# Optimization experiments

Hardware: AMD Instinct MI355X
Metric: run time of the kernel (lower is better)

## Reference

```python
import jax, jax.numpy as jnp
import numpy as np

B, N, F_IN, F_OUT = 8, 2048, 128, 64
ALPHA = 0.2  # LeakyReLU negative slope
NEG_INF = -9e15


def setup_inputs() -> dict:
    key = jax.random.key(0)
    k1, k2, k3, k4 = jax.random.split(key, 4)
    h = jax.random.normal(k1, (B, N, F_IN), dtype=jnp.float32)
    adj = jax.random.randint(k2, (B, N, N), 0, 2, dtype=jnp.int32)
    # xavier_uniform with gain=1.414 approximated by scaled normals (values are arbitrary params)
    W = jax.random.normal(k3, (F_IN, F_OUT), dtype=jnp.float32) * (1.414 * np.sqrt(2.0 / (F_IN + F_OUT)))
    a = jax.random.normal(k4, (2 * F_OUT, 1), dtype=jnp.float32) * (1.414 * np.sqrt(2.0 / (2 * F_OUT + 1)))
    return {"h": h, "adj": adj, "W": W, "a": a}


def reference(h, adj, W, a):
    # Wh: [B, N, F_out]
    Wh = jnp.einsum('bnf,fo->bno', h, W)
    Fo = W.shape[1]
    a1 = a[:Fo, 0]   # [F_out]
    a2 = a[Fo:, 0]   # [F_out]
    # e[b,i,j] = leakyrelu(Wh[b,i]@a1 + Wh[b,j]@a2)  (== cat(Wh_i,Wh_j)@a, same math, no N^2*2F blowup)
    e1 = jnp.einsum('bno,o->bn', Wh, a1)  # [B, N]
    e2 = jnp.einsum('bno,o->bn', Wh, a2)  # [B, N]
    e = e1[:, :, None] + e2[:, None, :]   # [B, N, N]
    e = jnp.where(e > 0, e, ALPHA * e)    # LeakyReLU
    e = jnp.where(adj > 0, e, NEG_INF)    # mask non-edges
    attention = jax.nn.softmax(e, axis=-1)
    # dropout is identity in inference mode (deterministic reference)
    h_prime = jnp.einsum('bij,bjo->bio', attention, Wh)  # [B, N, F_out]
    return jax.nn.elu(h_prime)  # concat=True branch
```

## Files before the change

kernel.cpp:

```cpp
#include <hip/hip_runtime.h>
#include <hip/hip_bf16.h>

#define BB 8
#define NN 2048
#define FIN 128
#define FO 64
#define ALPHA 0.2f

typedef __attribute__((ext_vector_type(8))) short bf16x8;
typedef __attribute__((ext_vector_type(4))) float f32x4;
typedef __attribute__((ext_vector_type(4))) int i32x4;

typedef __attribute__((address_space(1))) const void gvoid;
typedef __attribute__((address_space(3))) void lvoid;

__device__ inline void gl_lds16(const void* g, void* l) {
    __builtin_amdgcn_global_load_lds((gvoid*)g, (lvoid*)l, 16, 0, 0);
}

__device__ inline short f2bf(float x) {
    unsigned u = __float_as_uint(x);
    u += 0x7fffu + ((u >> 16) & 1u);
    return (short)(u >> 16);
}

__global__ __launch_bounds__(256) void wh_kernel(
    const float* __restrict__ h, const float* __restrict__ W,
    const float* __restrict__ a, float* __restrict__ e1, float* __restrict__ e2,
    short* __restrict__ whF)
{
    __shared__ float hs[32][FIN];
    const int r0 = blockIdx.x * 32;
    const int t = threadIdx.x;
    const float4* hsrc = (const float4*)(h + (size_t)r0 * FIN);
    float4* hdst = (float4*)(&hs[0][0]);
#pragma unroll
    for (int k = 0; k < 4; k++) hdst[t + 256 * k] = hsrc[t + 256 * k];
    __syncthreads();

    const int o = t & 63;
    const int wv = t >> 6;
    float acc[8];
#pragma unroll
    for (int rr = 0; rr < 8; rr++) acc[rr] = 0.f;

    for (int f = 0; f < FIN; f += 4) {
        const float w0 = W[(f + 0) * FO + o];
        const float w1 = W[(f + 1) * FO + o];
        const float w2 = W[(f + 2) * FO + o];
        const float w3 = W[(f + 3) * FO + o];
#pragma unroll
        for (int rr = 0; rr < 8; rr++) {
            float4 hv = *(const float4*)&hs[wv * 8 + rr][f];
            acc[rr] = fmaf(hv.x, w0, acc[rr]);
            acc[rr] = fmaf(hv.y, w1, acc[rr]);
            acc[rr] = fmaf(hv.z, w2, acc[rr]);
            acc[rr] = fmaf(hv.w, w3, acc[rr]);
        }
    }

    const int b   = r0 / NN;
    const int ib0 = r0 - b * NN;
    const int ibb = ib0 + wv * 8;
    const int jc  = ibb >> 5;
    const int qq  = (ibb >> 3) & 3;
    const int ot  = o >> 4, mm = o & 15;
    const int L   = mm + qq * 16;
    bf16x8 frag;
#pragma unroll
    for (int rr = 0; rr < 8; rr++) frag[rr] = f2bf(acc[rr]);
    *(bf16x8*)(whF + ((((size_t)(b * 64 + jc) * 4 + ot) * 64 + L) * 8)) = frag;

    const float a1 = a[o], a2 = a[FO + o];
#pragma unroll
    for (int rr = 0; rr < 8; rr++) {
        float v1 = acc[rr] * a1, v2 = acc[rr] * a2;
#pragma unroll
        for (int msk = 32; msk >= 1; msk >>= 1) {
            v1 += __shfl_xor(v1, msk, 64);
            v2 += __shfl_xor(v2, msk, 64);
        }
        if (o == 0) { e1[r0 + wv * 8 + rr] = v1; e2[r0 + wv * 8 + rr] = v2; }
    }
}

__global__ __launch_bounds__(256) void e2max_kernel(
    const float* __restrict__ e2, float* __restrict__ e2max)
{
    const int b = blockIdx.x;
    const int t = threadIdx.x;
    float m = -1e30f;
    for (int j = t; j < NN; j += 256) m = fmaxf(m, e2[b * NN + j]);
#pragma unroll
    for (int k = 32; k >= 1; k >>= 1) m = fmaxf(m, __shfl_xor(m, k, 64));
    __shared__ float red[4];
    if ((t & 63) == 0) red[t >> 6] = m;
    __syncthreads();
    if (t == 0) e2max[b] = fmaxf(fmaxf(red[0], red[1]), fmaxf(red[2], red[3]));
}

struct SMemS { int adj[16][260]; float e2[256]; };
struct SMemC { float comb[4][16][64]; float lsum[4][16]; };
union SMemU { SMemS s; SMemC c; };

__global__ __launch_bounds__(256) void attn_kernel(
    const int* __restrict__ adj, const float* __restrict__ e1,
    const float* __restrict__ e2, const float* __restrict__ e2max,
    const short* __restrict__ whF, float* __restrict__ out)
{
    __shared__ SMemU sm;
    const int t = threadIdx.x, w = t >> 6, lane = t & 63;
    const int m = lane & 15, q = lane >> 4;
    const int blk = blockIdx.x;
    const int b  = blk >> 7;
    const int i0 = (blk & 127) * 16;
    const int i  = i0 + m;

    const float e1v = e1[b * NN + i];
    float mi = e1v + e2max[b];
    mi = mi > 0.f ? mi : ALPHA * mi;

    const short* whFb = whF + (size_t)b * (64 * 4 * 64 * 8);
    const int* arow0 = adj + ((size_t)(b * NN + i0)) * NN + lane * 4;
    const float* e2g = e2 + b * NN + lane * 4;

    f32x4 acc0 = {0.f,0.f,0.f,0.f}, acc1 = acc0, acc2 = acc0, acc3 = acc0;
    float lsum = 0.f;

    for (int j0 = 0; j0 < NN; j0 += 256) {
#pragma unroll
        for (int k = 0; k < 4; k++) {
            const int r = w * 4 + k;
            gl_lds16(arow0 + (size_t)r * NN + j0, &sm.s.adj[r][0]);
        }
        if (w == 0) gl_lds16(e2g + j0, &sm.s.e2[0]);
        __syncthreads();

#pragma unroll
        for (int s2 = 0; s2 < 2; s2++) {
            const int col = w * 64 + s2 * 32 + q * 8;
            i32x4 a0 = *(const i32x4*)&sm.s.adj[m][col];
            i32x4 a1 = *(const i32x4*)&sm.s.adj[m][col + 4];
            f32x4 ev0 = *(const f32x4*)&sm.s.e2[col];
            f32x4 ev1 = *(const f32x4*)&sm.s.e2[col + 4];

            bf16x8 af;
#pragma unroll
            for (int jj = 0; jj < 8; jj++) {
                const int   av  = (jj < 4) ? a0[jj]      : a1[jj - 4];
                const float e2j = (jj < 4) ? ev0[jj]     : ev1[jj - 4];
                float e = e1v + e2j;
                e = e > 0.f ? e : ALPHA * e;
                const float pe = (av > 0) ? __expf(e - mi) : 0.f;
                lsum += pe;
                af[jj] = f2bf(pe);
            }

            const int jc = (j0 + w * 64 + s2 * 32) >> 5;
            const short* bfp = whFb + (size_t)jc * 2048 + lane * 8;
            bf16x8 b0 = *(const bf16x8*)(bfp);
            bf16x8 b1 = *(const bf16x8*)(bfp + 512);
            bf16x8 b2 = *(const bf16x8*)(bfp + 1024);
            bf16x8 b3 = *(const bf16x8*)(bfp + 1536);

            acc0 = __builtin_amdgcn_mfma_f32_16x16x32_bf16(af, b0, acc0, 0, 0, 0);
            acc1 = __builtin_amdgcn_mfma_f32_16x16x32_bf16(af, b1, acc1, 0, 0, 0);
            acc2 = __builtin_amdgcn_mfma_f32_16x16x32_bf16(af, b2, acc2, 0, 0, 0);
            acc3 = __builtin_amdgcn_mfma_f32_16x16x32_bf16(af, b3, acc3, 0, 0, 0);
        }
        __syncthreads();
    }

    lsum += __shfl_xor(lsum, 16, 64);
    lsum += __shfl_xor(lsum, 32, 64);
    if (q == 0) sm.c.lsum[w][m] = lsum;
#pragma unroll
    for (int ot = 0; ot < 4; ot++) {
        f32x4 av = (ot == 0) ? acc0 : (ot == 1) ? acc1 : (ot == 2) ? acc2 : acc3;
#pragma unroll
        for (int reg = 0; reg < 4; reg++)
            sm.c.comb[w][q * 4 + reg][ot * 16 + m] = av[reg];
    }
    __syncthreads();

    const int row = t >> 4, c0 = (t & 15) * 4;
    f32x4 sum = *(const f32x4*)&sm.c.comb[0][row][c0];
#pragma unroll
    for (int ww = 1; ww < 4; ww++) {
        f32x4 sv = *(const f32x4*)&sm.c.comb[ww][row][c0];
        sum.x += sv.x; sum.y += sv.y; sum.z += sv.z; sum.w += sv.w;
    }
    float l = sm.c.lsum[0][row] + sm.c.lsum[1][row] + sm.c.lsum[2][row] + sm.c.lsum[3][row];
    l = fmaxf(l, 1e-30f);
    const float rl = 1.f / l;
    float vr[4] = { sum.x * rl, sum.y * rl, sum.z * rl, sum.w * rl };
    f32x4 res;
#pragma unroll
    for (int kk = 0; kk < 4; kk++)
        res[kk] = vr[kk] > 0.f ? vr[kk] : (__expf(vr[kk]) - 1.f);
    *(f32x4*)&out[((size_t)(b * NN + i0 + row)) * FO + c0] = res;
}

extern "C" void kernel_launch(void* const* d_in, const int* in_sizes, int n_in,
                              void* d_out, int out_size, void* d_ws, size_t ws_size,
                              hipStream_t stream) {
    const float* h   = (const float*)d_in[0];
    const int*   adj = (const int*)d_in[1];
    const float* W   = (const float*)d_in[2];
    const float* a   = (const float*)d_in[3];
    float* out = (float*)d_out;

    char* ws = (char*)d_ws;
    short* whF = (short*)ws;
    size_t off = (size_t)BB * 64 * 4 * 64 * 8 * sizeof(short);
    float* e1  = (float*)(ws + off);  off += (size_t)BB * NN * 4;
    float* e2  = (float*)(ws + off);  off += (size_t)BB * NN * 4;
    float* e2m = (float*)(ws + off);

    wh_kernel<<<(BB * NN) / 32, 256, 0, stream>>>(h, W, a, e1, e2, whF);
    e2max_kernel<<<BB, 256, 0, stream>>>(e2, e2m);
    attn_kernel<<<BB * (NN / 16), 256, 0, stream>>>(adj, e1, e2, e2m, whF, out);
}
```

Measured before the change: 217.2 us.

## Pipeline per-wave adjacency loads with async LDS ring and branchless exp2 masking

The attention kernel now gives each wave its own contiguous 512-column slice of adjacency. That slice streams through a 4-deep per-wave LDS ring using global_load_lds and vmcnt waits, replacing block-wide __syncthreads per tile. The LDS layout is XOR-swizzled to avoid bank conflicts. Masking is done branchlessly with exp2 and a large additive offset on the adjacency value, bf16 conversion becomes truncation via perm, and the row sum is computed with an extra MFMA against a vector of ones. Risks: the truncating bf16 conversion loses precision, the mask trick relies on adj being 0 or 1, and the fixed vmcnt counts must match the number of issued loads.

Measured after the change: 222.3 us. +2.4%, slower.

```diff
diff --git a/kernel.cpp b/kernel.cpp
--- a/kernel.cpp
+++ b/kernel.cpp
@@ -99,81 +99,108 @@
     if (t == 0) e2max[b] = fmaxf(fmaxf(red[0], red[1]), fmaxf(red[2], red[3]));
 }
 
-struct SMemS { int adj[16][260]; float e2[256]; };
+struct SMemS {
+    int   adjs[4][4][16][8][4];
+    float e2s[4][512];
+};
 struct SMemC { float comb[4][16][64]; float lsum[4][16]; };
 union SMemU { SMemS s; SMemC c; };
 
-__global__ __launch_bounds__(256) void attn_kernel(
+#define WAITVM_(n) asm volatile("s_waitcnt vmcnt(" #n ")" ::: "memory")
+#define WAITVM(n) WAITVM_(n)
+
+#define STAGE(k) do { \
+    gl_lds16(asrc0 + (size_t)(k) * 32, &ladj[(k) & 3][0][0][0]); \
+    gl_lds16(asrc1 + (size_t)(k) * 32, &ladj[(k) & 3][8][0][0]); \
+} while (0)
+
+#define STEPC(k, VM) do { \
+    WAITVM(VM); \
+    i32x4 va0 = *(const i32x4*)&ladj[(k) & 3][m][u0][0]; \
+    i32x4 va1 = *(const i32x4*)&ladj[(k) & 3][m][u1][0]; \
+    f32x4 ev0 = *(const f32x4*)&le2[(k) * 32 + q * 8]; \
+    f32x4 ev1 = *(const f32x4*)&le2[(k) * 32 + q * 8 + 4]; \
+    const short* bfp = whFw + (size_t)(k) * 2048; \
+    bf16x8 wb0 = *(const bf16x8*)(bfp); \
+    bf16x8 wb1 = *(const bf16x8*)(bfp + 512); \
+    bf16x8 wb2 = *(const bf16x8*)(bfp + 1024); \
+    bf16x8 wb3 = *(const bf16x8*)(bfp + 1536); \
+    float pe[8]; \
+    _Pragma("unroll") \
+    for (int jj = 0; jj < 8; jj++) { \
+        const int   av = (jj < 4) ? va0[jj] : va1[jj - 4]; \
+        const float ej = (jj < 4) ? ev0[jj] : ev1[jj - 4]; \
+        const float s  = fmaf(ej, L2E, E1v); \
+        const float tt = fmaf(ALPHA, fminf(s, 0.f), fmaxf(s, 0.f)) - MiB; \
+        pe[jj] = __builtin_amdgcn_exp2f(fmaf((float)av, 4000.0f, tt)); \
+    } \
+    union { unsigned u[4]; bf16x8 v; } au; \
+    _Pragma("unroll") \
+    for (int jj = 0; jj < 4; jj++) \
+        au.u[jj] = __builtin_amdgcn_perm(__float_as_uint(pe[2 * jj + 1]), \
+                                         __float_as_uint(pe[2 * jj]), 0x07060302u); \
+    acc0 = __builtin_amdgcn_mfma_f32_16x16x32_bf16(au.v, wb0, acc0, 0, 0, 0); \
+    acc1 = __builtin_amdgcn_mfma_f32_16x16x32_bf16(au.v, wb1, acc1, 0, 0, 0); \
+    acc2 = __builtin_amdgcn_mfma_f32_16x16x32_bf16(au.v, wb2, acc2, 0, 0, 0); \
+    acc3 = __builtin_amdgcn_mfma_f32_16x16x32_bf16(au.v, wb3, acc3, 0, 0, 0); \
+    acc4 = __builtin_amdgcn_mfma_f32_16x16x32_bf16(au.v, ones, acc4, 0, 0, 0); \
+} while (0)
+
+__global__ __launch_bounds__(256, 4) void attn_kernel(
     const int* __restrict__ adj, const float* __restrict__ e1,
     const float* __restrict__ e2, const float* __restrict__ e2max,
     const short* __restrict__ whF, float* __restrict__ out)
 {
-    __shared__ SMemU sm;
+    __shared__ __align__(16) SMemU sm;
     const int t = threadIdx.x, w = t >> 6, lane = t & 63;
     const int m = lane & 15, q = lane >> 4;
     const int blk = blockIdx.x;
-    const int b  = blk >> 7;
-    const int i0 = (blk & 127) * 16;
-    const int i  = i0 + m;
-
-    const float e1v = e1[b * NN + i];
-    float mi = e1v + e2max[b];
-    mi = mi > 0.f ? mi : ALPHA * mi;
-
-    const short* whFb = whF + (size_t)b * (64 * 4 * 64 * 8);
-    const int* arow0 = adj + ((size_t)(b * NN + i0)) * NN + lane * 4;
-    const float* e2g = e2 + b * NN + lane * 4;
-
-    f32x4 acc0 = {0.f,0.f,0.f,0.f}, acc1 = acc0, acc2 = acc0, acc3 = acc0;
-    float lsum = 0.f;
-
-    for (int j0 = 0; j0 < NN; j0 += 256) {
-#pragma unroll
-        for (int k = 0; k < 4; k++) {
-            const int r = w * 4 + k;
-            gl_lds16(arow0 + (size_t)r * NN + j0, &sm.s.adj[r][0]);
-        }
-        if (w == 0) gl_lds16(e2g + j0, &sm.s.e2[0]);
-        __syncthreads();
-
-#pragma unroll
-        for (int s2 = 0; s2 < 2; s2++) {
-            const int col = w * 64 + s2 * 32 + q * 8;
-            i32x4 a0 = *(const i32x4*)&sm.s.adj[m][col];
-            i32x4 a1 = *(const i32x4*)&sm.s.adj[m][col + 4];
-            f32x4 ev0 = *(const f32x4*)&sm.s.e2[col];
-            f32x4 ev1 = *(const f32x4*)&sm.s.e2[col + 4];
-
-            bf16x8 af;
-#pragma unroll
-            for (int jj = 0; jj < 8; jj++) {
-                const int   av  = (jj < 4) ? a0[jj]      : a1[jj - 4];
-                const float e2j = (jj < 4) ? ev0[jj]     : ev1[jj - 4];
-                float e = e1v + e2j;
-                e = e > 0.f ? e : ALPHA * e;
-                const float pe = (av > 0) ? __expf(e - mi) : 0.f;
-                lsum += pe;
-                af[jj] = f2bf(pe);
-            }
-
-            const int jc = (j0 + w * 64 + s2 * 32) >> 5;
-            const short* bfp = whFb + (size_t)jc * 2048 + lane * 8;
-            bf16x8 b0 = *(const bf16x8*)(bfp);
-            bf16x8 b1 = *(const bf16x8*)(bfp + 512);
-            bf16x8 b2 = *(const bf16x8*)(bfp + 1024);
-            bf16x8 b3 = *(const bf16x8*)(bfp + 1536);
-
-            acc0 = __builtin_amdgcn_mfma_f32_16x16x32_bf16(af, b0, acc0, 0, 0, 0);
-            acc1 = __builtin_amdgcn_mfma_f32_16x16x32_bf16(af, b1, acc1, 0, 0, 0);
-            acc2 = __builtin_amdgcn_mfma_f32_16x16x32_bf16(af, b2, acc2, 0, 0, 0);
-            acc3 = __builtin_amdgcn_mfma_f32_16x16x32_bf16(af, b3, acc3, 0, 0, 0);
-        }
-        __syncthreads();
-    }
-
-    lsum += __shfl_xor(lsum, 16, 64);
-    lsum += __shfl_xor(lsum, 32, 64);
-    if (q == 0) sm.c.lsum[w][m] = lsum;
+    const int b = blk >> 7, i0 = (blk & 127) * 16;
+
+    const float L2E = 1.4426950408889634f;
+    const float e1v = e1[b * NN + i0 + m];
+    float mr = e1v + e2max[b];
+    mr = mr > 0.f ? mr : ALPHA * mr;
+    const float E1v = e1v * L2E;
+    const float MiB = mr * L2E + 4000.0f;
+
+    const int l8 = lane >> 3, c7 = lane & 7;
+    const int csw = (c7 ^ l8) * 4;
+    const int* asrc0 = adj + ((size_t)(b * NN + i0 + l8)) * NN + w * 512 + csw;
+    const int* asrc1 = asrc0 + (size_t)8 * NN;
+    int (*ladj)[16][8][4] = sm.s.adjs[w];
+    float* le2 = sm.s.e2s[w];
+    const float* e2src = e2 + b * NN + w * 512 + lane * 4;
+
+    const short* whFw = whF + (size_t)b * (64 * 4 * 64 * 8)
+                            + (size_t)(w * 16) * 2048 + lane * 8;
+
+    f32x4 acc0 = {0.f,0.f,0.f,0.f}, acc1 = acc0, acc2 = acc0, acc3 = acc0, acc4 = acc0;
+    bf16x8 ones;
+#pragma unroll
+    for (int jj = 0; jj < 8; jj++) ones[jj] = (short)0x3F80;
+
+    const int u0 = (q * 2) ^ (m & 7);
+    const int u1 = u0 ^ 1;
+
+    gl_lds16(e2src,       &le2[0]);
+    gl_lds16(e2src + 256, &le2[256]);
+    STAGE(0); STAGE(1); STAGE(2);
+
+#pragma unroll 1
+    for (int k = 0; k < 13; k++) {
+        STAGE(k + 3);
+        STEPC(k, 6);
+    }
+    STEPC(13, 4);
+    STEPC(14, 2);
+    STEPC(15, 0);
+
+    __syncthreads();
+    if (m == 0) {
+#pragma unroll
+        for (int r = 0; r < 4; r++) sm.c.lsum[w][q * 4 + r] = acc4[r];
+    }
 #pragma unroll
     for (int ot = 0; ot < 4; ot++) {
         f32x4 av = (ot == 0) ? acc0 : (ot == 1) ? acc1 : (ot == 2) ? acc2 : acc3;
@@ -193,8 +220,8 @@
     float l = sm.c.lsum[0][row] + sm.c.lsum[1][row] + sm.c.lsum[2][row] + sm.c.lsum[3][row];
     l = fmaxf(l, 1e-30f);
     const float rl = 1.f / l;
+    f32x4 res;
     float vr[4] = { sum.x * rl, sum.y * rl, sum.z * rl, sum.w * rl };
-    f32x4 res;
 #pragma unroll
     for (int kk = 0; kk < 4; kk++)
         res[kk] = vr[kk] > 0.f ? vr[kk] : (__expf(vr[kk]) - 1.f);
```
